# Kernel tuning notes

Measured on AMD Instinct MI355X. Metric: run time of the kernel, lower is better.

## Reference

```python
import jax, jax.numpy as jnp
import numpy as np

I, J, K = 64, 8192, 128  # agents, batch, comm_channels


def setup_inputs() -> dict:
    key = jax.random.key(0)
    ks = jax.random.split(key, 7)
    s = 1.0 / np.sqrt(K)  # roughly torch Linear init scale
    return {
        "x": jax.random.normal(ks[0], (I, J, K), dtype=jnp.float32),
        "Wv": jax.random.normal(ks[1], (K, K), dtype=jnp.float32) * s,
        "bv": jax.random.normal(ks[2], (K,), dtype=jnp.float32) * s,
        "Wq": jax.random.normal(ks[3], (K, K), dtype=jnp.float32) * s,
        "bq": jax.random.normal(ks[4], (K,), dtype=jnp.float32) * s,
        "Wk": jax.random.normal(ks[5], (K, K), dtype=jnp.float32) * s,
        "bk": jax.random.normal(ks[6], (K,), dtype=jnp.float32) * s,
        "index": 3,
    }


def reference(x, Wv, bv, Wq, bq, Wk, bk, index):
    # x: [I, J, K] = torch.cat(input_comms, 0)
    v = jnp.einsum('ijk,ck->ijc', x, Wv) + bv          # [I, J, K]
    q = jnp.einsum('ijk,ck->ijc', x, Wq) + bq          # [I, J, K]
    k = jnp.einsum('jk,ck->jc', x[index], Wk) + bk     # [J, K] (gather one agent)
    att = jnp.einsum('ijk,jk->ij', q, k)               # [I, J]
    att = jax.nn.softmax(att, axis=0)                  # softmax over agents
    features = jnp.einsum('ij,ijk->jk', att, v)        # [J, K]
    return features
```

## Files before the change

### kernel.cpp

```cpp
#include <hip/hip_runtime.h>

#define NI 64
#define NJ 8192
#define NK 128
#define GMAIN 2048

#define WS_M    0
#define WS_WVT  16384
#define WS_D    32768
#define WS_KQ   32896

__global__ __launch_bounds__(128) void precompute_kernel(
    const float* __restrict__ Wv, const float* __restrict__ Wq,
    const float* __restrict__ Wk, const float* __restrict__ bk,
    float* __restrict__ ws)
{
    const int b = blockIdx.x;
    const int k = threadIdx.x;
    float macc = 0.f, dacc = 0.f;
    for (int c = 0; c < NK; ++c) {
        float wq = Wq[c*NK + k];
        macc += Wk[c*NK + b] * wq;
        if (b == 0) dacc += bk[c] * wq;
    }
    ws[WS_M + b*NK + k] = macc;
    ws[WS_WVT + b*NK + k] = Wv[k*NK + b];
    if (b == 0) ws[WS_D + k] = dacc;
}

__global__ __launch_bounds__(256) void kq_kernel(
    const float* __restrict__ x, const int* __restrict__ pIdx,
    const float* __restrict__ ws, float* __restrict__ kqout)
{
    const int tid = threadIdx.x;
    const int k2  = tid & 63;
    const int wv  = tid >> 6;
    const int j0  = blockIdx.x * 16 + wv * 4;
    const int idx = *pIdx;
    const float* __restrict__ M  = ws + WS_M;
    const float* __restrict__ x3 = x + (size_t)idx * NJ * NK;

    const float* r0 = x3 + (size_t)(j0+0)*NK;
    const float* r1 = x3 + (size_t)(j0+1)*NK;
    const float* r2 = x3 + (size_t)(j0+2)*NK;
    const float* r3 = x3 + (size_t)(j0+3)*NK;

    float d0 = ws[WS_D + 2*k2], d1 = ws[WS_D + 2*k2 + 1];
    float2 acc[4];
#pragma unroll
    for (int jj = 0; jj < 4; ++jj) { acc[jj].x = d0; acc[jj].y = d1; }

#pragma unroll 2
    for (int kp = 0; kp < NK; kp += 4) {
        float4 x0 = *(const float4*)(r0 + kp);
        float4 x1 = *(const float4*)(r1 + kp);
        float4 x2 = *(const float4*)(r2 + kp);
        float4 x3v = *(const float4*)(r3 + kp);
        float2 m0 = *(const float2*)(M + (kp+0)*NK + 2*k2);
        float2 m1 = *(const float2*)(M + (kp+1)*NK + 2*k2);
        float2 m2 = *(const float2*)(M + (kp+2)*NK + 2*k2);
        float2 m3 = *(const float2*)(M + (kp+3)*NK + 2*k2);
        acc[0].x += x0.x*m0.x + x0.y*m1.x + x0.z*m2.x + x0.w*m3.x;
        acc[0].y += x0.x*m0.y + x0.y*m1.y + x0.z*m2.y + x0.w*m3.y;
        acc[1].x += x1.x*m0.x + x1.y*m1.x + x1.z*m2.x + x1.w*m3.x;
        acc[1].y += x1.x*m0.y + x1.y*m1.y + x1.z*m2.y + x1.w*m3.y;
        acc[2].x += x2.x*m0.x + x2.y*m1.x + x2.z*m2.x + x2.w*m3.x;
        acc[2].y += x2.x*m0.y + x2.y*m1.y + x2.z*m2.y + x2.w*m3.y;
        acc[3].x += x3v.x*m0.x + x3v.y*m1.x + x3v.z*m2.x + x3v.w*m3.x;
        acc[3].y += x3v.x*m0.y + x3v.y*m1.y + x3v.z*m2.y + x3v.w*m3.y;
    }
#pragma unroll
    for (int jj = 0; jj < 4; ++jj)
        *(float2*)(kqout + (size_t)(j0+jj)*NK + 2*k2) = acc[jj];
}

__global__ __launch_bounds__(256, 4) void att_y_kernel(
    const float* __restrict__ x, const float* __restrict__ kq,
    float* __restrict__ y)
{
    __shared__ float att_s[NI];
    __shared__ float y_part[4*NK];

    const int tid  = threadIdx.x;
    const int lane = tid & 63;
    const int wave = tid >> 6;
    const int half = lane >> 5;
    const int lq   = lane & 31;
    const int k0   = lq * 4;
    const int ibase = wave*16 + half*8;
    const size_t ISTEP = (size_t)NJ * NK;

    const float* xb = x + (size_t)ibase * ISTEP + k0;

    float4 A[8], B[8];

    auto issue = [&](int j, float4 (&buf)[8]) {
        const float* p = xb + (size_t)j * NK;
#pragma unroll
        for (int t = 0; t < 8; ++t)
            buf[t] = *(const float4*)(p + (size_t)t * ISTEP);
    };
    auto lkq = [&](int j) -> float4 {
        return *(const float4*)(kq + (size_t)j * NK + k0);
    };

    auto process = [&](int j, float4 (&buf)[8], float4 kqv) {
        float p[8];
#pragma unroll
        for (int t = 0; t < 8; ++t)
            p[t] = buf[t].x*kqv.x + buf[t].y*kqv.y + buf[t].z*kqv.z + buf[t].w*kqv.w;
#pragma unroll
        for (int t = 0; t < 8; ++t) {
            p[t] += __shfl_xor(p[t], 1);
            p[t] += __shfl_xor(p[t], 2);
            p[t] += __shfl_xor(p[t], 4);
            p[t] += __shfl_xor(p[t], 8);
            p[t] += __shfl_xor(p[t], 16);
        }
#pragma unroll
        for (int t = 0; t < 8; ++t)
            if (lq == t) att_s[ibase + t] = p[t];
        __syncthreads();
        if (tid < NI) {
            float v = att_s[tid];
            float m = v;
            m = fmaxf(m, __shfl_xor(m, 1));  m = fmaxf(m, __shfl_xor(m, 2));
            m = fmaxf(m, __shfl_xor(m, 4));  m = fmaxf(m, __shfl_xor(m, 8));
            m = fmaxf(m, __shfl_xor(m, 16)); m = fmaxf(m, __shfl_xor(m, 32));
            float e = __expf(v - m);
            float s = e;
            s += __shfl_xor(s, 1);  s += __shfl_xor(s, 2);
            s += __shfl_xor(s, 4);  s += __shfl_xor(s, 8);
            s += __shfl_xor(s, 16); s += __shfl_xor(s, 32);
            att_s[tid] = e / s;
        }
        __syncthreads();
        float4 acc = make_float4(0.f, 0.f, 0.f, 0.f);
#pragma unroll
        for (int t = 0; t < 8; ++t) {
            float a = att_s[ibase + t];
            acc.x += a * buf[t].x; acc.y += a * buf[t].y;
            acc.z += a * buf[t].z; acc.w += a * buf[t].w;
        }
        acc.x += __shfl_xor(acc.x, 32); acc.y += __shfl_xor(acc.y, 32);
        acc.z += __shfl_xor(acc.z, 32); acc.w += __shfl_xor(acc.w, 32);
        if (half == 0)
            *(float4*)&y_part[wave*NK + k0] = acc;
        __syncthreads();
        if (tid < NK) {
            float s = y_part[tid] + y_part[NK+tid] + y_part[2*NK+tid] + y_part[3*NK+tid];
            y[(size_t)j * NK + tid] = s;
        }
    };

    const int j0 = blockIdx.x;
    issue(j0, A);             float4 kqA = lkq(j0);
    issue(j0 + GMAIN, B);     float4 kqB = lkq(j0 + GMAIN);
    process(j0, A, kqA);
    issue(j0 + 2*GMAIN, A);   kqA = lkq(j0 + 2*GMAIN);
    process(j0 + GMAIN, B, kqB);
    issue(j0 + 3*GMAIN, B);   kqB = lkq(j0 + 3*GMAIN);
    process(j0 + 2*GMAIN, A, kqA);
    process(j0 + 3*GMAIN, B, kqB);
}

__global__ __launch_bounds__(256) void feat_kernel(
    float* __restrict__ yio, const float* __restrict__ bv,
    const float* __restrict__ ws)
{
    const int tid = threadIdx.x;
    const int k2  = tid & 63;
    const int wv  = tid >> 6;
    const int j0  = blockIdx.x * 16 + wv * 4;
    const float* __restrict__ W = ws + WS_WVT;

    const float* r0 = yio + (size_t)(j0+0)*NK;
    const float* r1 = yio + (size_t)(j0+1)*NK;
    const float* r2 = yio + (size_t)(j0+2)*NK;
    const float* r3 = yio + (size_t)(j0+3)*NK;

    float b0 = bv[2*k2], b1 = bv[2*k2 + 1];
    float2 acc[4];
#pragma unroll
    for (int jj = 0; jj < 4; ++jj) { acc[jj].x = b0; acc[jj].y = b1; }

#pragma unroll 2
    for (int kp = 0; kp < NK; kp += 4) {
        float4 x0 = *(const float4*)(r0 + kp);
        float4 x1 = *(const float4*)(r1 + kp);
        float4 x2 = *(const float4*)(r2 + kp);
        float4 x3v = *(const float4*)(r3 + kp);
        float2 m0 = *(const float2*)(W + (kp+0)*NK + 2*k2);
        float2 m1 = *(const float2*)(W + (kp+1)*NK + 2*k2);
        float2 m2 = *(const float2*)(W + (kp+2)*NK + 2*k2);
        float2 m3 = *(const float2*)(W + (kp+3)*NK + 2*k2);
        acc[0].x += x0.x*m0.x + x0.y*m1.x + x0.z*m2.x + x0.w*m3.x;
        acc[0].y += x0.x*m0.y + x0.y*m1.y + x0.z*m2.y + x0.w*m3.y;
        acc[1].x += x1.x*m0.x + x1.y*m1.x + x1.z*m2.x + x1.w*m3.x;
        acc[1].y += x1.x*m0.y + x1.y*m1.y + x1.z*m2.y + x1.w*m3.y;
        acc[2].x += x2.x*m0.x + x2.y*m1.x + x2.z*m2.x + x2.w*m3.x;
        acc[2].y += x2.x*m0.y + x2.y*m1.y + x2.z*m2.y + x2.w*m3.y;
        acc[3].x += x3v.x*m0.x + x3v.y*m1.x + x3v.z*m2.x + x3v.w*m3.x;
        acc[3].y += x3v.x*m0.y + x3v.y*m1.y + x3v.z*m2.y + x3v.w*m3.y;
    }
#pragma unroll
    for (int jj = 0; jj < 4; ++jj)
        *(float2*)(yio + (size_t)(j0+jj)*NK + 2*k2) = acc[jj];
}

extern "C" void kernel_launch(void* const* d_in, const int* in_sizes, int n_in,
                              void* d_out, int out_size, void* d_ws, size_t ws_size,
                              hipStream_t stream) {
    const float* x  = (const float*)d_in[0];
    const float* Wv = (const float*)d_in[1];
    const float* bv = (const float*)d_in[2];
    const float* Wq = (const float*)d_in[3];
    const float* bq = (const float*)d_in[4];  (void)bq;
    const float* Wk = (const float*)d_in[5];
    const float* bk = (const float*)d_in[6];
    const int*  idx = (const int*)d_in[7];
    float* ws  = (float*)d_ws;
    float* out = (float*)d_out;

    precompute_kernel<<<NK, NK, 0, stream>>>(Wv, Wq, Wk, bk, ws);
    kq_kernel<<<NJ/16, 256, 0, stream>>>(x, idx, ws, ws + WS_KQ);
    att_y_kernel<<<GMAIN, 256, 0, stream>>>(x, ws + WS_KQ, out);
    feat_kernel<<<NJ/16, 256, 0, stream>>>(out, bv, ws);
}
```

Measured before the change: 109.0 us.

## Map one wave per batch row with online softmax, removing block barriers

The attention kernel now gives each wave a single batch column j, with each half-wave walking 32 agents using an online (running max/sum) softmax. The two halves are merged with a cross-lane shuffle, so shared memory and all __syncthreads are gone. This is meant to remove the per-row block barriers and LDS traffic that serialized the four waves. The cost is extra exp/rescale work per chunk and a larger grid of smaller blocks.

```diff
diff --git a/kernel.cpp b/kernel.cpp
--- a/kernel.cpp
+++ b/kernel.cpp
@@ -3,7 +3,6 @@
 #define NI 64
 #define NJ 8192
 #define NK 128
-#define GMAIN 2048
 
 #define WS_M    0
 #define WS_WVT  16384
@@ -78,33 +77,29 @@
     const float* __restrict__ x, const float* __restrict__ kq,
     float* __restrict__ y)
 {
-    __shared__ float att_s[NI];
-    __shared__ float y_part[4*NK];
-
     const int tid  = threadIdx.x;
     const int lane = tid & 63;
     const int wave = tid >> 6;
     const int half = lane >> 5;
     const int lq   = lane & 31;
     const int k0   = lq * 4;
-    const int ibase = wave*16 + half*8;
+    const int j    = blockIdx.x * 4 + wave;
     const size_t ISTEP = (size_t)NJ * NK;
 
-    const float* xb = x + (size_t)ibase * ISTEP + k0;
+    const float* xb = x + (size_t)(half * 32) * ISTEP + (size_t)j * NK + k0;
+    const float4 kqv = *(const float4*)(kq + (size_t)j * NK + k0);
 
     float4 A[8], B[8];
-
-    auto issue = [&](int j, float4 (&buf)[8]) {
-        const float* p = xb + (size_t)j * NK;
+    auto ld = [&](int r0, float4 (&buf)[8]) {
 #pragma unroll
         for (int t = 0; t < 8; ++t)
-            buf[t] = *(const float4*)(p + (size_t)t * ISTEP);
+            buf[t] = *(const float4*)(xb + (size_t)(r0 + t) * ISTEP);
     };
-    auto lkq = [&](int j) -> float4 {
-        return *(const float4*)(kq + (size_t)j * NK + k0);
-    };
-
-    auto process = [&](int j, float4 (&buf)[8], float4 kqv) {
+
+    float m = -3.0e38f, s = 0.f;
+    float4 yacc = make_float4(0.f, 0.f, 0.f, 0.f);
+
+    auto proc = [&](float4 (&buf)[8]) {
         float p[8];
 #pragma unroll
         for (int t = 0; t < 8; ++t)
@@ -117,51 +112,49 @@
             p[t] += __shfl_xor(p[t], 8);
             p[t] += __shfl_xor(p[t], 16);
         }
-#pragma unroll
-        for (int t = 0; t < 8; ++t)
-            if (lq == t) att_s[ibase + t] = p[t];
-        __syncthreads();
-        if (tid < NI) {
-            float v = att_s[tid];
-            float m = v;
-            m = fmaxf(m, __shfl_xor(m, 1));  m = fmaxf(m, __shfl_xor(m, 2));
-            m = fmaxf(m, __shfl_xor(m, 4));  m = fmaxf(m, __shfl_xor(m, 8));
-            m = fmaxf(m, __shfl_xor(m, 16)); m = fmaxf(m, __shfl_xor(m, 32));
-            float e = __expf(v - m);
-            float s = e;
-            s += __shfl_xor(s, 1);  s += __shfl_xor(s, 2);
-            s += __shfl_xor(s, 4);  s += __shfl_xor(s, 8);
-            s += __shfl_xor(s, 16); s += __shfl_xor(s, 32);
-            att_s[tid] = e / s;
+        float cm = fmaxf(fmaxf(fmaxf(p[0],p[1]), fmaxf(p[2],p[3])),
+                         fmaxf(fmaxf(p[4],p[5]), fmaxf(p[6],p[7])));
+        float mn = fmaxf(m, cm);
+        float sc = __expf(m - mn);
+        s *= sc;
+        yacc.x *= sc; yacc.y *= sc; yacc.z *= sc; yacc.w *= sc;
+#pragma unroll
+        for (int t = 0; t < 8; ++t) {
+            float e = __expf(p[t] - mn);
+            s += e;
+            yacc.x += e * buf[t].x; yacc.y += e * buf[t].y;
+            yacc.z += e * buf[t].z; yacc.w += e * buf[t].w;
         }
-        __syncthreads();
-        float4 acc = make_float4(0.f, 0.f, 0.f, 0.f);
-#pragma unroll
-        for (int t = 0; t < 8; ++t) {
-            float a = att_s[ibase + t];
-            acc.x += a * buf[t].x; acc.y += a * buf[t].y;
-            acc.z += a * buf[t].z; acc.w += a * buf[t].w;
-        }
-        acc.x += __shfl_xor(acc.x, 32); acc.y += __shfl_xor(acc.y, 32);
-        acc.z += __shfl_xor(acc.z, 32); acc.w += __shfl_xor(acc.w, 32);
-        if (half == 0)
-            *(float4*)&y_part[wave*NK + k0] = acc;
-        __syncthreads();
-        if (tid < NK) {
-            float s = y_part[tid] + y_part[NK+tid] + y_part[2*NK+tid] + y_part[3*NK+tid];
-            y[(size_t)j * NK + tid] = s;
-        }
+        m = mn;
     };
 
-    const int j0 = blockIdx.x;
-    issue(j0, A);             float4 kqA = lkq(j0);
-    issue(j0 + GMAIN, B);     float4 kqB = lkq(j0 + GMAIN);
-    process(j0, A, kqA);
-    issue(j0 + 2*GMAIN, A);   kqA = lkq(j0 + 2*GMAIN);
-    process(j0 + GMAIN, B, kqB);
-    issue(j0 + 3*GMAIN, B);   kqB = lkq(j0 + 3*GMAIN);
-    process(j0 + 2*GMAIN, A, kqA);
-    process(j0 + 3*GMAIN, B, kqB);
+    ld(0, A);
+    ld(8, B);
+    proc(A);
+    ld(16, A);
+    proc(B);
+    ld(24, B);
+    proc(A);
+    proc(B);
+
+    float m_o = __shfl_xor(m, 32);
+    float s_o = __shfl_xor(s, 32);
+    float4 y_o;
+    y_o.x = __shfl_xor(yacc.x, 32);
+    y_o.y = __shfl_xor(yacc.y, 32);
+    y_o.z = __shfl_xor(yacc.z, 32);
+    y_o.w = __shfl_xor(yacc.w, 32);
+    float M  = fmaxf(m, m_o);
+    float es = __expf(m - M), eo = __expf(m_o - M);
+    float S  = s * es + s_o * eo;
+    float inv = 1.f / S;
+    float4 yf;
+    yf.x = (yacc.x * es + y_o.x * eo) * inv;
+    yf.y = (yacc.y * es + y_o.y * eo) * inv;
+    yf.z = (yacc.z * es + y_o.z * eo) * inv;
+    yf.w = (yacc.w * es + y_o.w * eo) * inv;
+    if (half == 0)
+        *(float4*)(y + (size_t)j * NK + k0) = yf;
 }
 
 __global__ __launch_bounds__(256) void feat_kernel(
@@ -224,6 +217,6 @@
 
     precompute_kernel<<<NK, NK, 0, stream>>>(Wv, Wq, Wk, bk, ws);
     kq_kernel<<<NJ/16, 256, 0, stream>>>(x, idx, ws, ws + WS_KQ);
-    att_y_kernel<<<GMAIN, 256, 0, stream>>>(x, ws + WS_KQ, out);
+    att_y_kernel<<<NJ/4, 256, 0, stream>>>(x, ws + WS_KQ, out);
     feat_kernel<<<NJ/16, 256, 0, stream>>>(out, bv, ws);
 }
```

Result: slower. 115.8 us (+6.2%).

## Fuse attention and output projection with per-wave online softmax over agents

Applied to the files above, without the earlier changes.

Replaces the attention kernel and the separate output-projection kernel with one kernel. Each block handles 8 batch rows, and each wave walks its 16 agents with an online softmax (running max and sum, exp2 with log2e folded into kq) plus a triple-buffered nontemporal load pipeline. Per-wave partial results are merged through shared memory, and the Wv projection is applied in the same kernel. This removes three block-wide barriers per row and the round trip of y through global memory. In exchange it adds more registers per thread and an extra rescale multiply for every agent.

```diff
diff --git a/kernel.cpp b/kernel.cpp
--- a/kernel.cpp
+++ b/kernel.cpp
@@ -3,7 +3,10 @@
 #define NI 64
 #define NJ 8192
 #define NK 128
-#define GMAIN 2048
+#define JB 8
+#define LOG2E 1.44269504088896340736f
+
+typedef float f32x4 __attribute__((ext_vector_type(4)));
 
 #define WS_M    0
 #define WS_WVT  16384
@@ -70,142 +73,138 @@
         acc[3].y += x3v.x*m0.y + x3v.y*m1.y + x3v.z*m2.y + x3v.w*m3.y;
     }
 #pragma unroll
-    for (int jj = 0; jj < 4; ++jj)
-        *(float2*)(kqout + (size_t)(j0+jj)*NK + 2*k2) = acc[jj];
-}
-
-__global__ __launch_bounds__(256, 4) void att_y_kernel(
-    const float* __restrict__ x, const float* __restrict__ kq,
-    float* __restrict__ y)
+    for (int jj = 0; jj < 4; ++jj) {
+        float2 o; o.x = acc[jj].x * LOG2E; o.y = acc[jj].y * LOG2E;
+        *(float2*)(kqout + (size_t)(j0+jj)*NK + 2*k2) = o;
+    }
+}
+
+__global__ __launch_bounds__(256, 4) void att_y_feat_kernel(
+    const float* __restrict__ x, const float* __restrict__ ws,
+    const float* __restrict__ bv, float* __restrict__ out)
 {
-    __shared__ float att_s[NI];
-    __shared__ float y_part[4*NK];
+    __shared__ float yacc_s[4][JB][NK];
+    __shared__ float y_s[JB][NK];
+    __shared__ float m_s[4][JB], s_s[4][JB];
 
     const int tid  = threadIdx.x;
     const int lane = tid & 63;
-    const int wave = tid >> 6;
-    const int half = lane >> 5;
+    const int w    = tid >> 6;
+    const int h    = lane >> 5;
     const int lq   = lane & 31;
     const int k0   = lq * 4;
-    const int ibase = wave*16 + half*8;
+    const int j0   = blockIdx.x * JB;
     const size_t ISTEP = (size_t)NJ * NK;
 
-    const float* xb = x + (size_t)ibase * ISTEP + k0;
-
-    float4 A[8], B[8];
-
-    auto issue = [&](int j, float4 (&buf)[8]) {
-        const float* p = xb + (size_t)j * NK;
-#pragma unroll
-        for (int t = 0; t < 8; ++t)
-            buf[t] = *(const float4*)(p + (size_t)t * ISTEP);
+    const float* __restrict__ kq = ws + WS_KQ;
+
+    f32x4 kqv[4];
+#pragma unroll
+    for (int q = 0; q < 4; ++q)
+        kqv[q] = *(const f32x4*)(kq + (size_t)(j0 + 2*q + h)*NK + k0);
+
+    const float* xb = x + (size_t)(w*16) * ISTEP + (size_t)j0 * NK
+                        + (size_t)h * NK + k0;
+
+    f32x4 buf[3][4];
+    auto issue = [&](int i, int slot) {
+#pragma unroll
+        for (int q = 0; q < 4; ++q)
+            buf[slot][q] = __builtin_nontemporal_load(
+                (const f32x4*)(xb + (size_t)i * ISTEP + q * 256));
     };
-    auto lkq = [&](int j) -> float4 {
-        return *(const float4*)(kq + (size_t)j * NK + k0);
+
+    float m[4] = {-3.0e38f, -3.0e38f, -3.0e38f, -3.0e38f};
+    float s[4] = {0.f, 0.f, 0.f, 0.f};
+    f32x4 yacc[4] = {};
+
+    auto process = [&](int slot) {
+        float p[4];
+#pragma unroll
+        for (int q = 0; q < 4; ++q) {
+            f32x4 b = buf[slot][q];
+            p[q] = b[0]*kqv[q][0] + b[1]*kqv[q][1] + b[2]*kqv[q][2] + b[3]*kqv[q][3];
+        }
+#pragma unroll
+        for (int q = 0; q < 4; ++q) {
+            p[q] += __shfl_xor(p[q], 1);
+            p[q] += __shfl_xor(p[q], 2);
+            p[q] += __shfl_xor(p[q], 4);
+            p[q] += __shfl_xor(p[q], 8);
+            p[q] += __shfl_xor(p[q], 16);
+        }
+#pragma unroll
+        for (int q = 0; q < 4; ++q) {
+            float mn = fmaxf(m[q], p[q]);
+            float sc = __builtin_amdgcn_exp2f(m[q] - mn);
+            float e  = __builtin_amdgcn_exp2f(p[q] - mn);
+            s[q] = s[q] * sc + e;
+            f32x4 b = buf[slot][q];
+            yacc[q][0] = yacc[q][0]*sc + e*b[0];
+            yacc[q][1] = yacc[q][1]*sc + e*b[1];
+            yacc[q][2] = yacc[q][2]*sc + e*b[2];
+            yacc[q][3] = yacc[q][3]*sc + e*b[3];
+            m[q] = mn;
+        }
     };
 
-    auto process = [&](int j, float4 (&buf)[8], float4 kqv) {
-        float p[8];
-#pragma unroll
-        for (int t = 0; t < 8; ++t)
-            p[t] = buf[t].x*kqv.x + buf[t].y*kqv.y + buf[t].z*kqv.z + buf[t].w*kqv.w;
-#pragma unroll
-        for (int t = 0; t < 8; ++t) {
-            p[t] += __shfl_xor(p[t], 1);
-            p[t] += __shfl_xor(p[t], 2);
-            p[t] += __shfl_xor(p[t], 4);
-            p[t] += __shfl_xor(p[t], 8);
-            p[t] += __shfl_xor(p[t], 16);
-        }
-#pragma unroll
-        for (int t = 0; t < 8; ++t)
-            if (lq == t) att_s[ibase + t] = p[t];
-        __syncthreads();
-        if (tid < NI) {
-            float v = att_s[tid];
-            float m = v;
-            m = fmaxf(m, __shfl_xor(m, 1));  m = fmaxf(m, __shfl_xor(m, 2));
-            m = fmaxf(m, __shfl_xor(m, 4));  m = fmaxf(m, __shfl_xor(m, 8));
-            m = fmaxf(m, __shfl_xor(m, 16)); m = fmaxf(m, __shfl_xor(m, 32));
-            float e = __expf(v - m);
-            float s = e;
-            s += __shfl_xor(s, 1);  s += __shfl_xor(s, 2);
-            s += __shfl_xor(s, 4);  s += __shfl_xor(s, 8);
-            s += __shfl_xor(s, 16); s += __shfl_xor(s, 32);
-            att_s[tid] = e / s;
-        }
-        __syncthreads();
-        float4 acc = make_float4(0.f, 0.f, 0.f, 0.f);
-#pragma unroll
-        for (int t = 0; t < 8; ++t) {
-            float a = att_s[ibase + t];
-            acc.x += a * buf[t].x; acc.y += a * buf[t].y;
-            acc.z += a * buf[t].z; acc.w += a * buf[t].w;
-        }
-        acc.x += __shfl_xor(acc.x, 32); acc.y += __shfl_xor(acc.y, 32);
-        acc.z += __shfl_xor(acc.z, 32); acc.w += __shfl_xor(acc.w, 32);
-        if (half == 0)
-            *(float4*)&y_part[wave*NK + k0] = acc;
-        __syncthreads();
-        if (tid < NK) {
-            float s = y_part[tid] + y_part[NK+tid] + y_part[2*NK+tid] + y_part[3*NK+tid];
-            y[(size_t)j * NK + tid] = s;
-        }
-    };
-
-    const int j0 = blockIdx.x;
-    issue(j0, A);             float4 kqA = lkq(j0);
-    issue(j0 + GMAIN, B);     float4 kqB = lkq(j0 + GMAIN);
-    process(j0, A, kqA);
-    issue(j0 + 2*GMAIN, A);   kqA = lkq(j0 + 2*GMAIN);
-    process(j0 + GMAIN, B, kqB);
-    issue(j0 + 3*GMAIN, B);   kqB = lkq(j0 + 3*GMAIN);
-    process(j0 + 2*GMAIN, A, kqA);
-    process(j0 + 3*GMAIN, B, kqB);
-}
-
-__global__ __launch_bounds__(256) void feat_kernel(
-    float* __restrict__ yio, const float* __restrict__ bv,
-    const float* __restrict__ ws)
-{
-    const int tid = threadIdx.x;
-    const int k2  = tid & 63;
-    const int wv  = tid >> 6;
-    const int j0  = blockIdx.x * 16 + wv * 4;
-    const float* __restrict__ W = ws + WS_WVT;
-
-    const float* r0 = yio + (size_t)(j0+0)*NK;
-    const float* r1 = yio + (size_t)(j0+1)*NK;
-    const float* r2 = yio + (size_t)(j0+2)*NK;
-    const float* r3 = yio + (size_t)(j0+3)*NK;
-
-    float b0 = bv[2*k2], b1 = bv[2*k2 + 1];
-    float2 acc[4];
-#pragma unroll
-    for (int jj = 0; jj < 4; ++jj) { acc[jj].x = b0; acc[jj].y = b1; }
-
-#pragma unroll 2
-    for (int kp = 0; kp < NK; kp += 4) {
-        float4 x0 = *(const float4*)(r0 + kp);
-        float4 x1 = *(const float4*)(r1 + kp);
-        float4 x2 = *(const float4*)(r2 + kp);
-        float4 x3v = *(const float4*)(r3 + kp);
-        float2 m0 = *(const float2*)(W + (kp+0)*NK + 2*k2);
-        float2 m1 = *(const float2*)(W + (kp+1)*NK + 2*k2);
-        float2 m2 = *(const float2*)(W + (kp+2)*NK + 2*k2);
-        float2 m3 = *(const float2*)(W + (kp+3)*NK + 2*k2);
-        acc[0].x += x0.x*m0.x + x0.y*m1.x + x0.z*m2.x + x0.w*m3.x;
-        acc[0].y += x0.x*m0.y + x0.y*m1.y + x0.z*m2.y + x0.w*m3.y;
-        acc[1].x += x1.x*m0.x + x1.y*m1.x + x1.z*m2.x + x1.w*m3.x;
-        acc[1].y += x1.x*m0.y + x1.y*m1.y + x1.z*m2.y + x1.w*m3.y;
-        acc[2].x += x2.x*m0.x + x2.y*m1.x + x2.z*m2.x + x2.w*m3.x;
-        acc[2].y += x2.x*m0.y + x2.y*m1.y + x2.z*m2.y + x2.w*m3.y;
-        acc[3].x += x3v.x*m0.x + x3v.y*m1.x + x3v.z*m2.x + x3v.w*m3.x;
-        acc[3].y += x3v.x*m0.y + x3v.y*m1.y + x3v.z*m2.y + x3v.w*m3.y;
-    }
-#pragma unroll
-    for (int jj = 0; jj < 4; ++jj)
-        *(float2*)(yio + (size_t)(j0+jj)*NK + 2*k2) = acc[jj];
+    issue(0, 0); issue(1, 1); issue(2, 2);
+#pragma unroll
+    for (int i = 0; i < 16; ++i) {
+        process(i % 3);
+        if (i + 3 < 16) issue(i + 3, i % 3);
+    }
+
+#pragma unroll
+    for (int q = 0; q < 4; ++q)
+        *(f32x4*)&yacc_s[w][2*q + h][k0] = yacc[q];
+    if (lq == 0) {
+#pragma unroll
+        for (int q = 0; q < 4; ++q) {
+            m_s[w][2*q + h] = m[q];
+            s_s[w][2*q + h] = s[q];
+        }
+    }
+    __syncthreads();
+
+    const int jj = tid >> 5;
+    const int c0 = (tid & 31) * 4;
+    {
+        float mM = fmaxf(fmaxf(m_s[0][jj], m_s[1][jj]),
+                         fmaxf(m_s[2][jj], m_s[3][jj]));
+        float coef[4];
+        float denom = 0.f;
+#pragma unroll
+        for (int wv = 0; wv < 4; ++wv) {
+            float c = __builtin_amdgcn_exp2f(m_s[wv][jj] - mM);
+            coef[wv] = c;
+            denom += c * s_s[wv][jj];
+        }
+        float inv = 1.f / denom;
+        f32x4 yv = {};
+#pragma unroll
+        for (int wv = 0; wv < 4; ++wv) {
+            f32x4 t = *(const f32x4*)&yacc_s[wv][jj][c0];
+            yv[0] += coef[wv] * t[0]; yv[1] += coef[wv] * t[1];
+            yv[2] += coef[wv] * t[2]; yv[3] += coef[wv] * t[3];
+        }
+        yv[0] *= inv; yv[1] *= inv; yv[2] *= inv; yv[3] *= inv;
+        *(f32x4*)&y_s[jj][c0] = yv;
+    }
+    __syncthreads();
+
+    {
+        const float* __restrict__ WvT = ws + WS_WVT;
+        f32x4 acc = *(const f32x4*)(bv + c0);
+#pragma unroll 4
+        for (int kp = 0; kp < NK; ++kp) {
+            float yk = y_s[jj][kp];
+            f32x4 wv4 = *(const f32x4*)(WvT + (size_t)kp * NK + c0);
+            acc[0] += yk * wv4[0]; acc[1] += yk * wv4[1];
+            acc[2] += yk * wv4[2]; acc[3] += yk * wv4[3];
+        }
+        *(f32x4*)(out + (size_t)(j0 + jj) * NK + c0) = acc;
+    }
 }
 
 extern "C" void kernel_launch(void* const* d_in, const int* in_sizes, int n_in,
@@ -224,6 +223,5 @@
 
     precompute_kernel<<<NK, NK, 0, stream>>>(Wv, Wq, Wk, bk, ws);
     kq_kernel<<<NJ/16, 256, 0, stream>>>(x, idx, ws, ws + WS_KQ);
-    att_y_kernel<<<GMAIN, 256, 0, stream>>>(x, ws + WS_KQ, out);
-    feat_kernel<<<NJ/16, 256, 0, stream>>>(out, bv, ws);
-}
+    att_y_feat_kernel<<<NJ/JB, 256, 0, stream>>>(x, ws, bv, out);
+}
```

New measurement: 173.6 us. +59.2%, slower.
